# Kernel optimization log

Measured on AMD Instinct MI355X. Metric: run time of the kernel, lower is better.

Reference implementation:

```python
import jax, jax.numpy as jnp
import numpy as np

B = 8388608
TRANSLATION_WEIGHT = 1.0
ROTATION_WEIGHT = 1.0


def setup_inputs() -> dict:
    key = jax.random.key(0)
    k1, k2 = jax.random.split(key)
    prediction = jax.random.normal(k1, (B, 7), dtype=jnp.float32)
    target = jax.random.normal(k2, (B, 7), dtype=jnp.float32)
    return {"prediction": prediction, "target": target}


def _geodesic_loss(q_pred, q_tgt):
    # scipy R.from_quat normalizes quaternions; relative rotation angle
    # magnitude(q_pred^-1 * q_tgt) = 2 * arccos(|<q_pred_hat, q_tgt_hat>|), in [0, pi]
    qp = q_pred / jnp.linalg.norm(q_pred, axis=-1, keepdims=True)
    qt = q_tgt / jnp.linalg.norm(q_tgt, axis=-1, keepdims=True)
    dot = jnp.abs(jnp.sum(qp * qt, axis=-1))
    angle = 2.0 * jnp.arccos(jnp.clip(dot, 0.0, 1.0))
    return jnp.mean(angle * angle)


def reference(prediction, target):
    t_pred, t_tgt = prediction[:, :3], target[:, :3]
    q_pred, q_tgt = prediction[:, 3:], target[:, 3:]
    translation_loss = jnp.mean((t_pred - t_tgt) ** 2)
    rotation_loss = _geodesic_loss(q_pred, q_tgt)
    return TRANSLATION_WEIGHT * translation_loss + ROTATION_WEIGHT * rotation_loss
```

## Files before the change

### kernel.cpp

```cpp
#include <hip/hip_runtime.h>


#define TILE_F4 1792
#define BLOCK 256

__global__ __launch_bounds__(BLOCK) void trl_partial_kernel(
    const float* __restrict__ pred,
    const float* __restrict__ targ,
    float* __restrict__ partial,
    int ntiles,
    int ngroups,
    float inv3B,
    float invB)
{
    const float4* __restrict__ p4 = (const float4*)pred;
    const float4* __restrict__ t4 = (const float4*)targ;

    __shared__ float4 sp[TILE_F4];
    __shared__ float4 st[TILE_F4];

    const int tid = threadIdx.x;

    float tsum = 0.0f;
    float rsum = 0.0f;

    for (int tile = blockIdx.x; tile < ntiles; tile += gridDim.x) {
        const int base = tile * TILE_F4;

#pragma unroll
        for (int j = 0; j < 7; ++j) {
            const int idx = j * BLOCK + tid;
            sp[idx] = p4[base + idx];
            st[idx] = t4[base + idx];
        }
        __syncthreads();

        float4 pa[7], ta[7];
#pragma unroll
        for (int k = 0; k < 7; ++k) pa[k] = sp[7 * tid + k];
#pragma unroll
        for (int k = 0; k < 7; ++k) ta[k] = st[7 * tid + k];

        const float* pv = (const float*)pa;
        const float* tv = (const float*)ta;
#pragma unroll
        for (int j = 0; j < 4; ++j) {
            const float* p = pv + 7 * j;
            const float* t = tv + 7 * j;

            float d0 = p[0] - t[0];
            float d1 = p[1] - t[1];
            float d2 = p[2] - t[2];
            tsum += d0 * d0 + d1 * d1 + d2 * d2;

            float np2 = p[3] * p[3] + p[4] * p[4] + p[5] * p[5] + p[6] * p[6];
            float nt2 = t[3] * t[3] + t[4] * t[4] + t[5] * t[5] + t[6] * t[6];
            float dot = p[3] * t[3] + p[4] * t[4] + p[5] * t[5] + p[6] * t[6];
            float c = fabsf(dot) * rsqrtf(np2 * nt2);
            c = fminf(c, 1.0f);
            float ang = 2.0f * acosf(c);
            rsum += ang * ang;
        }
        __syncthreads();
    }

    if (blockIdx.x == 0) {
        for (int g = ntiles * BLOCK + tid; g < ngroups; g += BLOCK) {
            float4 pa[7], ta[7];
            const long b = 7L * g;
#pragma unroll
            for (int k = 0; k < 7; ++k) pa[k] = p4[b + k];
#pragma unroll
            for (int k = 0; k < 7; ++k) ta[k] = t4[b + k];
            const float* pv = (const float*)pa;
            const float* tv = (const float*)ta;
#pragma unroll
            for (int j = 0; j < 4; ++j) {
                const float* p = pv + 7 * j;
                const float* t = tv + 7 * j;
                float d0 = p[0] - t[0], d1 = p[1] - t[1], d2 = p[2] - t[2];
                tsum += d0 * d0 + d1 * d1 + d2 * d2;
                float np2 = p[3]*p[3] + p[4]*p[4] + p[5]*p[5] + p[6]*p[6];
                float nt2 = t[3]*t[3] + t[4]*t[4] + t[5]*t[5] + t[6]*t[6];
                float dot = p[3]*t[3] + p[4]*t[4] + p[5]*t[5] + p[6]*t[6];
                float c = fminf(fabsf(dot) * rsqrtf(np2 * nt2), 1.0f);
                float ang = 2.0f * acosf(c);
                rsum += ang * ang;
            }
        }
    }

    float local = tsum * inv3B + rsum * invB;

#pragma unroll
    for (int off = 32; off > 0; off >>= 1)
        local += __shfl_down(local, off, 64);

    __shared__ float sdata[4];
    int lane = threadIdx.x & 63;
    int wave = threadIdx.x >> 6;
    if (lane == 0) sdata[wave] = local;
    __syncthreads();
    if (threadIdx.x == 0)
        partial[blockIdx.x] = sdata[0] + sdata[1] + sdata[2] + sdata[3];
}

__global__ __launch_bounds__(256) void trl_final_kernel(
    const float* __restrict__ partial, int n, float* __restrict__ out)
{
    float s = 0.0f;
    for (int i = threadIdx.x; i < n; i += 256) s += partial[i];
#pragma unroll
    for (int off = 32; off > 0; off >>= 1)
        s += __shfl_down(s, off, 64);
    __shared__ float sd[4];
    if ((threadIdx.x & 63) == 0) sd[threadIdx.x >> 6] = s;
    __syncthreads();
    if (threadIdx.x == 0) out[0] = sd[0] + sd[1] + sd[2] + sd[3];
}

extern "C" void kernel_launch(void* const* d_in, const int* in_sizes, int n_in,
                              void* d_out, int out_size, void* d_ws, size_t ws_size,
                              hipStream_t stream) {
    const float* pred = (const float*)d_in[0];
    const float* targ = (const float*)d_in[1];
    float* out = (float*)d_out;
    float* partial = (float*)d_ws;

    long long total = in_sizes[0];
    int B = (int)(total / 7);
    int ngroups = B / 4;
    int ntiles = ngroups / BLOCK;

    float invB  = 1.0f / (float)B;
    float inv3B = invB / 3.0f;

    const int grid = 2048;

    trl_partial_kernel<<<grid, BLOCK, 0, stream>>>(pred, targ, partial, ntiles, ngroups, inv3B, invB);
    trl_final_kernel<<<1, BLOCK, 0, stream>>>(partial, grid, out);
}
```

Before: 452.9 us.

## Stage tiles via direct global-to-LDS loads with halved tiles and higher occupancy

Replaces the register-staged global-to-shared copy with the AMD global_load_lds builtin, so data goes straight into LDS without passing through VGPRs. The tile is halved to 896 float4 (two samples per thread), reads from LDS use float2, and launch bounds request five blocks per CU to raise occupancy. The aim is better overlap and latency hiding on this memory-bound reduction. The cost is more tile iterations and barriers per block. Correctness depends on the builtin's per-lane addressing semantics and on the float2 tail path.

```diff
diff --git a/kernel.cpp b/kernel.cpp
--- a/kernel.cpp
+++ b/kernel.cpp
@@ -1,10 +1,17 @@
 #include <hip/hip_runtime.h>
 
 
-#define TILE_F4 1792
+#define TILE_F4 896
 #define BLOCK 256
 
-__global__ __launch_bounds__(BLOCK) void trl_partial_kernel(
+__device__ __forceinline__ void load_lds16(const float4* g, float4* l) {
+    __builtin_amdgcn_global_load_lds(
+        (__attribute__((address_space(1))) void*)g,
+        (__attribute__((address_space(3))) void*)l,
+        16, 0, 0);
+}
+
+__global__ __launch_bounds__(BLOCK, 5) void trl_partial_kernel(
     const float* __restrict__ pred,
     const float* __restrict__ targ,
     float* __restrict__ partial,
@@ -28,23 +35,30 @@
         const int base = tile * TILE_F4;
 
 #pragma unroll
-        for (int j = 0; j < 7; ++j) {
+        for (int j = 0; j < 3; ++j) {
             const int idx = j * BLOCK + tid;
-            sp[idx] = p4[base + idx];
-            st[idx] = t4[base + idx];
+            load_lds16(&p4[base + idx], &sp[idx]);
+            load_lds16(&t4[base + idx], &st[idx]);
+        }
+        if (tid < TILE_F4 - 3 * BLOCK) {
+            const int idx = 3 * BLOCK + tid;
+            load_lds16(&p4[base + idx], &sp[idx]);
+            load_lds16(&t4[base + idx], &st[idx]);
         }
         __syncthreads();
 
-        float4 pa[7], ta[7];
+        const float2* sp2 = (const float2*)sp;
+        const float2* st2 = (const float2*)st;
+        float2 pa[7], ta[7];
 #pragma unroll
-        for (int k = 0; k < 7; ++k) pa[k] = sp[7 * tid + k];
+        for (int k = 0; k < 7; ++k) pa[k] = sp2[7 * tid + k];
 #pragma unroll
-        for (int k = 0; k < 7; ++k) ta[k] = st[7 * tid + k];
+        for (int k = 0; k < 7; ++k) ta[k] = st2[7 * tid + k];
 
         const float* pv = (const float*)pa;
         const float* tv = (const float*)ta;
 #pragma unroll
-        for (int j = 0; j < 4; ++j) {
+        for (int j = 0; j < 2; ++j) {
             const float* p = pv + 7 * j;
             const float* t = tv + 7 * j;
 
@@ -65,17 +79,19 @@
     }
 
     if (blockIdx.x == 0) {
+        const float2* __restrict__ p2 = (const float2*)pred;
+        const float2* __restrict__ t2 = (const float2*)targ;
         for (int g = ntiles * BLOCK + tid; g < ngroups; g += BLOCK) {
-            float4 pa[7], ta[7];
+            float2 pa[7], ta[7];
             const long b = 7L * g;
 #pragma unroll
-            for (int k = 0; k < 7; ++k) pa[k] = p4[b + k];
+            for (int k = 0; k < 7; ++k) pa[k] = p2[b + k];
 #pragma unroll
-            for (int k = 0; k < 7; ++k) ta[k] = t4[b + k];
+            for (int k = 0; k < 7; ++k) ta[k] = t2[b + k];
             const float* pv = (const float*)pa;
             const float* tv = (const float*)ta;
 #pragma unroll
-            for (int j = 0; j < 4; ++j) {
+            for (int j = 0; j < 2; ++j) {
                 const float* p = pv + 7 * j;
                 const float* t = tv + 7 * j;
                 float d0 = p[0] - t[0], d1 = p[1] - t[1], d2 = p[2] - t[2];
@@ -129,7 +145,7 @@
 
     long long total = in_sizes[0];
     int B = (int)(total / 7);
-    int ngroups = B / 4;
+    int ngroups = B / 2;
     int ntiles = ngroups / BLOCK;
 
     float invB  = 1.0f / (float)B;
```

After: 447.0 us. No clear change (-1.3%).
